# Performance work log

Hardware: AMD Instinct MI355X
Metric: run time of the kernel (lower is better)

Reference implementation:

```python
import jax, jax.numpy as jnp
import numpy as np

BITS = 4        # int4_fullrange
NPACK = 8       # 32-bit container / 4-bit values
BLOCK = 64      # quantization group size (blocksize)
MASK = (1 << BITS) - 1


def _unpack(packed):
    """Unpack int32 words into NPACK 4-bit unsigned values along the last dim.
    packed: (..., P) int32 -> (..., P*NPACK) int32 in [0, 15]."""
    shifts = jnp.arange(NPACK, dtype=jnp.int32) * BITS  # (8,)
    vals = (packed[..., None] >> shifts) & MASK          # (..., P, 8)
    return vals.reshape(*packed.shape[:-1], packed.shape[-1] * NPACK)


def setup_inputs() -> dict:
    key = jax.random.key(0)
    k1, k2, k3, k4, k5 = jax.random.split(key, 5)
    tokens, in_f, out_f = 4096, 4096, 11008
    groups = in_f // BLOCK                      # 64
    x = jax.random.normal(k1, (tokens, in_f), jnp.float32)
    qweight = jax.random.randint(k2, (out_f, in_f // NPACK), 0, 2147483647, jnp.int32)
    qzeros = jax.random.randint(k3, (out_f, groups // NPACK), 0, 2147483647, jnp.int32)
    scales = jax.random.uniform(k4, (out_f, groups), jnp.float32, 0.001, 0.01)
    bias = jax.random.normal(k5, (out_f,), jnp.float32)
    return {"x": x, "qweight": qweight, "qzeros": qzeros, "scales": scales, "bias": bias}


def reference(x, qweight, qzeros, scales, bias):
    # Recover fp32 weight: w[o, g*BLOCK + b] = scales[o, g] * (w_int - zp[o, g])
    out_f, groups = scales.shape
    w_int = _unpack(qweight).astype(jnp.float32)           # (out, in)
    zp = _unpack(qzeros).astype(jnp.float32)               # (out, groups)
    w = (w_int.reshape(out_f, groups, BLOCK) - zp[:, :, None]) * scales[:, :, None]
    w = w.reshape(out_f, groups * BLOCK)                   # (out, in)
    # F.linear(x, w, bias)
    return x @ w.T + bias
```

## Files before the change

kernel.cpp:

```cpp
#include <hip/hip_runtime.h>
#include <stdint.h>

#define M_TOK 4096
#define K_IN  4096
#define N_OUT 11008
#define GROUPS 64
#define WPR 512

#define BM 256
#define BN 256
#define BK 64
#define TM (M_TOK / BM)
#define TN (N_OUT / BN)
#define NWG (TM * TN)
#define KTILES (K_IN / BK)

typedef __bf16 bf16x8 __attribute__((ext_vector_type(8)));
typedef float  f32x4  __attribute__((ext_vector_type(4)));

__device__ __forceinline__ uint16_t f2bf(float f) {
  uint32_t u = __float_as_uint(f);
  u += 0x7FFFu + ((u >> 16) & 1u);
  return (uint16_t)(u >> 16);
}

#define XBLK ((M_TOK * K_IN) / (256 * 8))
#define WBLK ((N_OUT * WPR) / (256 * 4))

__global__ __launch_bounds__(256) void prep(const float* __restrict__ x,
                                            const uint32_t* __restrict__ qw,
                                            const uint32_t* __restrict__ qz,
                                            const float* __restrict__ sc,
                                            uint16_t* __restrict__ xb,
                                            uint16_t* __restrict__ wb) {
  if (blockIdx.x < XBLK) {
    size_t i = ((size_t)blockIdx.x * 256 + threadIdx.x) * 8;
    const float4* p = (const float4*)(x + i);
    float4 a = p[0];
    float4 b = p[1];
    uint4 v;
    v.x = (uint32_t)f2bf(a.x) | ((uint32_t)f2bf(a.y) << 16);
    v.y = (uint32_t)f2bf(a.z) | ((uint32_t)f2bf(a.w) << 16);
    v.z = (uint32_t)f2bf(b.x) | ((uint32_t)f2bf(b.y) << 16);
    v.w = (uint32_t)f2bf(b.z) | ((uint32_t)f2bf(b.w) << 16);
    *(uint4*)(xb + i) = v;
  } else {
    int t = (blockIdx.x - XBLK) * 256 + threadIdx.x;
    int o  = t >> 7;
    int g  = (t & 127) >> 1;
    uint32_t zw = qz[o * (GROUPS / 8) + (g >> 3)];
    float zp = (float)((zw >> ((g & 7) * 4)) & 15u);
    float s = sc[o * GROUPS + g];
    float c = -s * zp;
    uint4 w4 = ((const uint4*)qw)[t];
    uint4* out = (uint4*)wb + (size_t)t * 4;
    uint32_t ws[4] = {w4.x, w4.y, w4.z, w4.w};
#pragma unroll
    for (int q = 0; q < 4; q++) {
      uint32_t w = ws[q];
      uint4 v;
      uint32_t r[4];
#pragma unroll
      for (int j = 0; j < 4; j++) {
        float f0 = (float)((w >> (8 * j)) & 15u);
        float f1 = (float)((w >> (8 * j + 4)) & 15u);
        r[j] = (uint32_t)f2bf(fmaf(f0, s, c)) | ((uint32_t)f2bf(fmaf(f1, s, c)) << 16);
      }
      v.x = r[0]; v.y = r[1]; v.z = r[2]; v.w = r[3];
      out[q] = v;
    }
  }
}

#define SBAR()   __builtin_amdgcn_s_barrier()
#define WAITV(n) asm volatile("s_waitcnt vmcnt(" #n ")" ::: "memory")

#define STAGE_A(buf, half, kt) do {                                            \
  _Pragma("unroll")                                                            \
  for (int c_ = 0; c_ < 2; c_++) {                                             \
    const int r_ = (half) * 128 + c_ * 64 + wave * 8;                          \
    __builtin_amdgcn_global_load_lds(                                          \
        (const __attribute__((address_space(1))) uint32_t*)(                   \
            gA + (size_t)r_ * K_IN + (size_t)(kt) * BK),                       \
        (__attribute__((address_space(3))) uint32_t*)(&As[(buf)][r_][0]),      \
        16, 0, 0);                                                             \
  } } while (0)

#define STAGE_B(buf, half, kt) do {                                            \
  _Pragma("unroll")                                                            \
  for (int c_ = 0; c_ < 2; c_++) {                                             \
    const int r_ = (half) * 128 + c_ * 64 + wave * 8;                          \
    __builtin_amdgcn_global_load_lds(                                          \
        (const __attribute__((address_space(1))) uint32_t*)(                   \
            gB + (size_t)r_ * K_IN + (size_t)(kt) * BK),                       \
        (__attribute__((address_space(3))) uint32_t*)(&Bs[(buf)][r_][0]),      \
        16, 0, 0);                                                             \
  } } while (0)

#define LOAD_A(buf, mh) do {                                                   \
  _Pragma("unroll")                                                            \
  for (int i2_ = 0; i2_ < 4; i2_++) {                                          \
    const int row_ = (mh) * 128 + wm * 64 + i2_ * 16 + col;                    \
    af[i2_][0] = *(const bf16x8*)&As[(buf)][row_][(quad ^ cs) << 3];           \
    af[i2_][1] = *(const bf16x8*)&As[(buf)][row_][((4 + quad) ^ cs) << 3];     \
  } } while (0)

#define LOAD_B(buf, nh) do {                                                   \
  _Pragma("unroll")                                                            \
  for (int j2_ = 0; j2_ < 2; j2_++) {                                          \
    const int row_ = (nh) * 128 + wn * 32 + j2_ * 16 + col;                    \
    bfr[(nh)][j2_][0] = *(const bf16x8*)&Bs[(buf)][row_][(quad ^ cs) << 3];    \
    bfr[(nh)][j2_][1] = *(const bf16x8*)&Bs[(buf)][row_][((4 + quad) ^ cs) << 3]; \
  } } while (0)

#define MMA(mh, nh) do {                                                       \
  __builtin_amdgcn_s_setprio(1);                                               \
  _Pragma("unroll")                                                            \
  for (int i2_ = 0; i2_ < 4; i2_++)                                            \
    _Pragma("unroll")                                                          \
    for (int j2_ = 0; j2_ < 2; j2_++) {                                        \
      acc[(mh)*4 + i2_][(nh)*2 + j2_] = __builtin_amdgcn_mfma_f32_16x16x32_bf16( \
          af[i2_][0], bfr[(nh)][j2_][0], acc[(mh)*4 + i2_][(nh)*2 + j2_], 0, 0, 0); \
      acc[(mh)*4 + i2_][(nh)*2 + j2_] = __builtin_amdgcn_mfma_f32_16x16x32_bf16( \
          af[i2_][1], bfr[(nh)][j2_][1], acc[(mh)*4 + i2_][(nh)*2 + j2_], 0, 0, 0); \
    }                                                                          \
  __builtin_amdgcn_s_setprio(0); } while (0)

__global__ __launch_bounds__(512, 2) void gemm_bf16(const uint16_t* __restrict__ A,
                                                    const uint16_t* __restrict__ B,
                                                    const float* __restrict__ bias,
                                                    float* __restrict__ C) {
  __shared__ __align__(16) uint16_t As[2][BM][BK];
  __shared__ __align__(16) uint16_t Bs[2][BN][BK];

  const int bid = blockIdx.x;
  const int wg  = (bid & 7) * (NWG / 8) + (bid >> 3);
  const int mt  = wg / TN;
  const int nt  = wg % TN;
  const size_t m0 = (size_t)mt * BM;
  const size_t n0 = (size_t)nt * BN;

  const int tid  = threadIdx.x;
  const int wave = tid >> 6;
  const int lane = tid & 63;
  const int wm   = wave >> 2;
  const int wn   = wave & 3;
  const int lrow = lane >> 3;
  const int lcol = lane & 7;
  const int col  = lane & 15;
  const int quad = lane >> 4;
  const int cs   = col & 7;

  const uint16_t* gA = A + (m0 + lrow) * K_IN + (size_t)((lcol ^ lrow) << 3);
  const uint16_t* gB = B + (n0 + lrow) * K_IN + (size_t)((lcol ^ lrow) << 3);

  f32x4 acc[8][4];
#pragma unroll
  for (int i = 0; i < 8; i++)
#pragma unroll
    for (int j = 0; j < 4; j++)
      acc[i][j] = (f32x4){0.f, 0.f, 0.f, 0.f};

  bf16x8 af[4][2];
  bf16x8 bfr[2][2][2];

  STAGE_A(0, 0, 0); STAGE_B(0, 1, 0); STAGE_B(0, 0, 0); STAGE_A(0, 1, 0);
  STAGE_A(1, 0, 1); STAGE_B(1, 1, 1);
  WAITV(6);
  SBAR();

  for (int it = 0; it < KTILES / 2 - 1; ++it) {
    const int kt = 2 * it;
    STAGE_B(1, 0, kt + 1);
    LOAD_A(0, 0); LOAD_B(0, 0);
    MMA(0, 0);
    SBAR();
    STAGE_A(1, 1, kt + 1);
    LOAD_B(0, 1);
    MMA(0, 1);
    WAITV(8);
    SBAR();
    STAGE_A(0, 0, kt + 2);
    LOAD_A(0, 1);
    MMA(1, 1);
    SBAR();
    STAGE_B(0, 1, kt + 2);
    MMA(1, 0);
    WAITV(6);
    SBAR();
    STAGE_B(0, 0, kt + 2);
    LOAD_A(1, 0); LOAD_B(1, 0);
    MMA(0, 0);
    SBAR();
    STAGE_A(0, 1, kt + 2);
    LOAD_B(1, 1);
    MMA(0, 1);
    WAITV(8);
    SBAR();
    STAGE_A(1, 0, kt + 3);
    LOAD_A(1, 1);
    MMA(1, 1);
    SBAR();
    STAGE_B(1, 1, kt + 3);
    MMA(1, 0);
    WAITV(6);
    SBAR();
  }

  STAGE_B(1, 0, KTILES - 1);
  LOAD_A(0, 0); LOAD_B(0, 0);
  MMA(0, 0);
  SBAR();
  STAGE_A(1, 1, KTILES - 1);
  LOAD_B(0, 1);
  MMA(0, 1);
  WAITV(8);
  SBAR();
  LOAD_A(0, 1);
  MMA(1, 1);
  SBAR();
  MMA(1, 0);
  WAITV(2);
  SBAR();
  LOAD_A(1, 0); LOAD_B(1, 0);
  MMA(0, 0);
  SBAR();
  LOAD_B(1, 1);
  MMA(0, 1);
  WAITV(0);
  SBAR();
  LOAD_A(1, 1);
  MMA(1, 1);
  SBAR();
  MMA(1, 0);

#pragma unroll
  for (int i = 0; i < 8; i++) {
    const int mrow = (int)m0 + (i >> 2) * 128 + wm * 64 + (i & 3) * 16 + quad * 4;
#pragma unroll
    for (int j = 0; j < 4; j++) {
      const int ncol = (int)n0 + (j >> 1) * 128 + wn * 32 + (j & 1) * 16 + col;
      const float bv = bias[ncol];
      float* out = C + (size_t)mrow * N_OUT + ncol;
#pragma unroll
      for (int r = 0; r < 4; r++)
        __builtin_nontemporal_store(acc[i][j][r] + bv, out + (size_t)r * N_OUT);
    }
  }
}

__global__ __launch_bounds__(256) void fallback_fused(const float* __restrict__ x,
                                                      const uint32_t* __restrict__ qw,
                                                      const uint32_t* __restrict__ qz,
                                                      const float* __restrict__ sc,
                                                      const float* __restrict__ bias,
                                                      float* __restrict__ out) {
  __shared__ float xs[K_IN];
  const int t = blockIdx.y;
  const int o = blockIdx.x * 256 + threadIdx.x;
  for (int i = threadIdx.x; i < K_IN; i += 256) xs[i] = x[(size_t)t * K_IN + i];
  __syncthreads();
  float acc = 0.f;
  const uint32_t* qwr = qw + (size_t)o * WPR;
  for (int g = 0; g < GROUPS; g++) {
    uint32_t zw = qz[o * (GROUPS / 8) + (g >> 3)];
    float zp = (float)((zw >> ((g & 7) * 4)) & 15u);
    float s = sc[o * GROUPS + g];
    float gacc = 0.f, gsum = 0.f;
    for (int w = 0; w < 8; w++) {
      uint32_t wv = qwr[g * 8 + w];
#pragma unroll
      for (int j = 0; j < 8; j++) {
        float xv = xs[g * 64 + w * 8 + j];
        gacc = fmaf((float)((wv >> (4 * j)) & 15u), xv, gacc);
        gsum += xv;
      }
    }
    acc += s * (gacc - zp * gsum);
  }
  out[(size_t)t * N_OUT + o] = acc + bias[o];
}

extern "C" void kernel_launch(void* const* d_in, const int* in_sizes, int n_in,
                              void* d_out, int out_size, void* d_ws, size_t ws_size,
                              hipStream_t stream) {
  (void)in_sizes; (void)n_in; (void)out_size;
  const float*    x    = (const float*)d_in[0];
  const uint32_t* qw   = (const uint32_t*)d_in[1];
  const uint32_t* qz   = (const uint32_t*)d_in[2];
  const float*    sc   = (const float*)d_in[3];
  const float*    bias = (const float*)d_in[4];
  float* out = (float*)d_out;

  const size_t xb_bytes = (size_t)M_TOK * K_IN * 2;
  const size_t wb_bytes = (size_t)N_OUT * K_IN * 2;

  if (ws_size >= xb_bytes + wb_bytes) {
    uint16_t* xb = (uint16_t*)d_ws;
    uint16_t* wb = (uint16_t*)((char*)d_ws + xb_bytes);
    prep<<<XBLK + WBLK, 256, 0, stream>>>(x, qw, qz, sc, xb, wb);
    gemm_bf16<<<NWG, 512, 0, stream>>>(xb, wb, bias, out);
  } else {
    fallback_fused<<<dim3(N_OUT / 256, M_TOK), 256, 0, stream>>>(x, qw, qz, sc, bias, out);
  }
}
```

Measured before the change: 574.6 us.

## Fuse int4 weight dequantization into GEMM B-tile staging

The separate pass that expanded the whole int4 weight to bf16 in global memory is removed; that kernel now converts only the activations. The GEMM loads packed qweight words, zero points and scales into registers, dequantizes them with FMAs, and writes bf16 into the swizzled LDS B tile. This avoids writing and re-reading the large bf16 weight buffer. In exchange, every M-tile redoes the dequantization inside the main loop, adding VALU work and register pressure. The explicit vmcnt waits are dropped and the A-tile async loads now rely on the compiler's waits for the B register loads.

```diff
diff --git a/kernel.cpp b/kernel.cpp
--- a/kernel.cpp
+++ b/kernel.cpp
@@ -25,55 +25,53 @@
 }
 
 #define XBLK ((M_TOK * K_IN) / (256 * 8))
-#define WBLK ((N_OUT * WPR) / (256 * 4))
-
-__global__ __launch_bounds__(256) void prep(const float* __restrict__ x,
-                                            const uint32_t* __restrict__ qw,
-                                            const uint32_t* __restrict__ qz,
-                                            const float* __restrict__ sc,
-                                            uint16_t* __restrict__ xb,
-                                            uint16_t* __restrict__ wb) {
-  if (blockIdx.x < XBLK) {
-    size_t i = ((size_t)blockIdx.x * 256 + threadIdx.x) * 8;
-    const float4* p = (const float4*)(x + i);
-    float4 a = p[0];
-    float4 b = p[1];
-    uint4 v;
-    v.x = (uint32_t)f2bf(a.x) | ((uint32_t)f2bf(a.y) << 16);
-    v.y = (uint32_t)f2bf(a.z) | ((uint32_t)f2bf(a.w) << 16);
-    v.z = (uint32_t)f2bf(b.x) | ((uint32_t)f2bf(b.y) << 16);
-    v.w = (uint32_t)f2bf(b.z) | ((uint32_t)f2bf(b.w) << 16);
-    *(uint4*)(xb + i) = v;
-  } else {
-    int t = (blockIdx.x - XBLK) * 256 + threadIdx.x;
-    int o  = t >> 7;
-    int g  = (t & 127) >> 1;
-    uint32_t zw = qz[o * (GROUPS / 8) + (g >> 3)];
-    float zp = (float)((zw >> ((g & 7) * 4)) & 15u);
-    float s = sc[o * GROUPS + g];
-    float c = -s * zp;
-    uint4 w4 = ((const uint4*)qw)[t];
-    uint4* out = (uint4*)wb + (size_t)t * 4;
-    uint32_t ws[4] = {w4.x, w4.y, w4.z, w4.w};
-#pragma unroll
-    for (int q = 0; q < 4; q++) {
-      uint32_t w = ws[q];
-      uint4 v;
-      uint32_t r[4];
-#pragma unroll
-      for (int j = 0; j < 4; j++) {
-        float f0 = (float)((w >> (8 * j)) & 15u);
-        float f1 = (float)((w >> (8 * j + 4)) & 15u);
-        r[j] = (uint32_t)f2bf(fmaf(f0, s, c)) | ((uint32_t)f2bf(fmaf(f1, s, c)) << 16);
-      }
-      v.x = r[0]; v.y = r[1]; v.z = r[2]; v.w = r[3];
-      out[q] = v;
-    }
-  }
+
+__global__ __launch_bounds__(256) void prep_x(const float* __restrict__ x,
+                                              uint16_t* __restrict__ xb) {
+  size_t i = ((size_t)blockIdx.x * 256 + threadIdx.x) * 8;
+  const float4* p = (const float4*)(x + i);
+  float4 a = p[0];
+  float4 b = p[1];
+  uint4 v;
+  v.x = (uint32_t)f2bf(a.x) | ((uint32_t)f2bf(a.y) << 16);
+  v.y = (uint32_t)f2bf(a.z) | ((uint32_t)f2bf(a.w) << 16);
+  v.z = (uint32_t)f2bf(b.x) | ((uint32_t)f2bf(b.y) << 16);
+  v.w = (uint32_t)f2bf(b.z) | ((uint32_t)f2bf(b.w) << 16);
+  *(uint4*)(xb + i) = v;
 }
 
 #define SBAR()   __builtin_amdgcn_s_barrier()
+#define SCHED0() __builtin_amdgcn_sched_barrier(0)
 #define WAITV(n) asm volatile("s_waitcnt vmcnt(" #n ")" ::: "memory")
+
+struct BB { uint32_t w0, w1, z0, z1; float s0, s1; };
+
+__device__ __forceinline__ uint4 deq8(uint32_t w, float s, float c) {
+  union { __bf16 h[8]; uint4 v; } u;
+#pragma unroll
+  for (int j = 0; j < 8; j++)
+    u.h[j] = (__bf16)fmaf((float)((w >> (4 * j)) & 15u), s, c);
+  return u.v;
+}
+
+#define ISSUE_B(bb, half, kt) do {                                             \
+  const int r0_ = (half) * 128 + wave * 8 + lrow;                              \
+  const size_t o0_ = n0 + r0_, o1_ = o0_ + 64;                                 \
+  bb.w0 = qw[o0_ * WPR + (size_t)(kt) * 8 + lcol];                             \
+  bb.w1 = qw[o1_ * WPR + (size_t)(kt) * 8 + lcol];                             \
+  bb.z0 = qz[o0_ * (GROUPS / 8) + ((kt) >> 3)];                                \
+  bb.z1 = qz[o1_ * (GROUPS / 8) + ((kt) >> 3)];                                \
+  bb.s0 = sc[o0_ * GROUPS + (kt)];                                             \
+  bb.s1 = sc[o1_ * GROUPS + (kt)];                                             \
+} while (0)
+
+#define DEQ_B(buf, half, bb, kt) do {                                          \
+  const int r0_ = (half) * 128 + wave * 8 + lrow;                              \
+  const float zp0_ = (float)((bb.z0 >> (((kt) & 7) * 4)) & 15u);               \
+  const float zp1_ = (float)((bb.z1 >> (((kt) & 7) * 4)) & 15u);               \
+  *(uint4*)&Bs[(buf)][r0_][bslot] = deq8(bb.w0, bb.s0, -bb.s0 * zp0_);         \
+  *(uint4*)&Bs[(buf)][r0_ + 64][bslot] = deq8(bb.w1, bb.s1, -bb.s1 * zp1_);    \
+} while (0)
 
 #define STAGE_A(buf, half, kt) do {                                            \
   _Pragma("unroll")                                                            \
@@ -86,17 +84,6 @@
         16, 0, 0);                                                             \
   } } while (0)
 
-#define STAGE_B(buf, half, kt) do {                                            \
-  _Pragma("unroll")                                                            \
-  for (int c_ = 0; c_ < 2; c_++) {                                             \
-    const int r_ = (half) * 128 + c_ * 64 + wave * 8;                          \
-    __builtin_amdgcn_global_load_lds(                                          \
-        (const __attribute__((address_space(1))) uint32_t*)(                   \
-            gB + (size_t)r_ * K_IN + (size_t)(kt) * BK),                       \
-        (__attribute__((address_space(3))) uint32_t*)(&Bs[(buf)][r_][0]),      \
-        16, 0, 0);                                                             \
-  } } while (0)
-
 #define LOAD_A(buf, mh) do {                                                   \
   _Pragma("unroll")                                                            \
   for (int i2_ = 0; i2_ < 4; i2_++) {                                          \
@@ -105,7 +92,7 @@
     af[i2_][1] = *(const bf16x8*)&As[(buf)][row_][((4 + quad) ^ cs) << 3];     \
   } } while (0)
 
-#define LOAD_B(buf, nh) do {                                                   \
+#define LDB_FRAG(buf, nh) do {                                                 \
   _Pragma("unroll")                                                            \
   for (int j2_ = 0; j2_ < 2; j2_++) {                                          \
     const int row_ = (nh) * 128 + wn * 32 + j2_ * 16 + col;                    \
@@ -126,10 +113,12 @@
     }                                                                          \
   __builtin_amdgcn_s_setprio(0); } while (0)
 
-__global__ __launch_bounds__(512, 2) void gemm_bf16(const uint16_t* __restrict__ A,
-                                                    const uint16_t* __restrict__ B,
-                                                    const float* __restrict__ bias,
-                                                    float* __restrict__ C) {
+__global__ __launch_bounds__(512, 2) void gemm_fused(const uint16_t* __restrict__ A,
+                                                     const uint32_t* __restrict__ qw,
+                                                     const uint32_t* __restrict__ qz,
+                                                     const float* __restrict__ sc,
+                                                     const float* __restrict__ bias,
+                                                     float* __restrict__ C) {
   __shared__ __align__(16) uint16_t As[2][BM][BK];
   __shared__ __align__(16) uint16_t Bs[2][BN][BK];
 
@@ -150,9 +139,9 @@
   const int col  = lane & 15;
   const int quad = lane >> 4;
   const int cs   = col & 7;
+  const int bslot = (lcol ^ lrow) << 3;
 
   const uint16_t* gA = A + (m0 + lrow) * K_IN + (size_t)((lcol ^ lrow) << 3);
-  const uint16_t* gB = B + (n0 + lrow) * K_IN + (size_t)((lcol ^ lrow) << 3);
 
   f32x4 acc[8][4];
 #pragma unroll
@@ -163,71 +152,73 @@
 
   bf16x8 af[4][2];
   bf16x8 bfr[2][2][2];
-
-  STAGE_A(0, 0, 0); STAGE_B(0, 1, 0); STAGE_B(0, 0, 0); STAGE_A(0, 1, 0);
-  STAGE_A(1, 0, 1); STAGE_B(1, 1, 1);
-  WAITV(6);
+  BB bb0, bb1, p0, p1;
+
+  STAGE_A(0, 0, 0); STAGE_A(0, 1, 0); STAGE_A(1, 0, 1);
+  ISSUE_B(p0, 0, 0); ISSUE_B(p1, 1, 0);
+  DEQ_B(0, 0, p0, 0); DEQ_B(0, 1, p1, 0);
+  ISSUE_B(p0, 1, 1);
+  DEQ_B(1, 1, p0, 1);
+  ISSUE_B(bb0, 0, 1);
   SBAR();
 
   for (int it = 0; it < KTILES / 2 - 1; ++it) {
     const int kt = 2 * it;
-    STAGE_B(1, 0, kt + 1);
-    LOAD_A(0, 0); LOAD_B(0, 0);
+    DEQ_B(1, 0, bb0, kt + 1);
+    LOAD_A(0, 0); LDB_FRAG(0, 0);
     MMA(0, 0);
     SBAR();
     STAGE_A(1, 1, kt + 1);
-    LOAD_B(0, 1);
+    ISSUE_B(bb1, 1, kt + 2); SCHED0();
+    LDB_FRAG(0, 1);
     MMA(0, 1);
-    WAITV(8);
     SBAR();
     STAGE_A(0, 0, kt + 2);
+    ISSUE_B(bb0, 0, kt + 2); SCHED0();
     LOAD_A(0, 1);
     MMA(1, 1);
     SBAR();
-    STAGE_B(0, 1, kt + 2);
+    DEQ_B(0, 1, bb1, kt + 2);
     MMA(1, 0);
-    WAITV(6);
-    SBAR();
-    STAGE_B(0, 0, kt + 2);
-    LOAD_A(1, 0); LOAD_B(1, 0);
+    SBAR();
+    DEQ_B(0, 0, bb0, kt + 2);
+    LOAD_A(1, 0); LDB_FRAG(1, 0);
     MMA(0, 0);
     SBAR();
     STAGE_A(0, 1, kt + 2);
-    LOAD_B(1, 1);
+    ISSUE_B(bb1, 1, kt + 3); SCHED0();
+    LDB_FRAG(1, 1);
     MMA(0, 1);
-    WAITV(8);
     SBAR();
     STAGE_A(1, 0, kt + 3);
+    ISSUE_B(bb0, 0, kt + 3); SCHED0();
     LOAD_A(1, 1);
     MMA(1, 1);
     SBAR();
-    STAGE_B(1, 1, kt + 3);
+    DEQ_B(1, 1, bb1, kt + 3);
     MMA(1, 0);
-    WAITV(6);
-    SBAR();
-  }
-
-  STAGE_B(1, 0, KTILES - 1);
-  LOAD_A(0, 0); LOAD_B(0, 0);
+    SBAR();
+  }
+
+  DEQ_B(1, 0, bb0, KTILES - 1);
+  LOAD_A(0, 0); LDB_FRAG(0, 0);
   MMA(0, 0);
   SBAR();
   STAGE_A(1, 1, KTILES - 1);
-  LOAD_B(0, 1);
+  LDB_FRAG(0, 1);
   MMA(0, 1);
-  WAITV(8);
   SBAR();
   LOAD_A(0, 1);
   MMA(1, 1);
   SBAR();
   MMA(1, 0);
-  WAITV(2);
-  SBAR();
-  LOAD_A(1, 0); LOAD_B(1, 0);
+  WAITV(0);
+  SBAR();
+  LOAD_A(1, 0); LDB_FRAG(1, 0);
   MMA(0, 0);
   SBAR();
-  LOAD_B(1, 1);
+  LDB_FRAG(1, 1);
   MMA(0, 1);
-  WAITV(0);
   SBAR();
   LOAD_A(1, 1);
   MMA(1, 1);
@@ -293,13 +284,11 @@
   float* out = (float*)d_out;
 
   const size_t xb_bytes = (size_t)M_TOK * K_IN * 2;
-  const size_t wb_bytes = (size_t)N_OUT * K_IN * 2;
-
-  if (ws_size >= xb_bytes + wb_bytes) {
+
+  if (ws_size >= xb_bytes) {
     uint16_t* xb = (uint16_t*)d_ws;
-    uint16_t* wb = (uint16_t*)((char*)d_ws + xb_bytes);
-    prep<<<XBLK + WBLK, 256, 0, stream>>>(x, qw, qz, sc, xb, wb);
-    gemm_bf16<<<NWG, 512, 0, stream>>>(xb, wb, bias, out);
+    prep_x<<<XBLK, 256, 0, stream>>>(x, xb);
+    gemm_fused<<<NWG, 512, 0, stream>>>(xb, qw, qz, sc, bias, out);
   } else {
     fallback_fused<<<dim3(N_OUT / 256, M_TOK), 256, 0, stream>>>(x, qw, qz, sc, bias, out);
   }
```

Result: slower. 679.4 us (+18.2%).
